# Performance work log

Measured on AMD Instinct MI355X. Metric: run time of the kernel, lower is better.

## Reference

```python
import jax, jax.numpy as jnp
import numpy as np

N, B, S, E, D, L, H, OUT = 16384, 32, 512, 262144, 256, 4, 4, 768
DH = D // H
ATOM_VOCABS = [119, 9, 12, 12, 10, 6, 9, 2, 2]
BOND_VOCABS = [22, 6, 2]
BN_EPS = 1e-5


def bn(x, g, b):
    # BatchNorm1d over nodes (training-mode statistics, deterministic)
    mu = x.mean(0)
    var = ((x - mu) ** 2).mean(0)
    return (x - mu) * jax.lax.rsqrt(var + BN_EPS) * g + b


def setup_inputs():
    key = jax.random.key(0)
    ks = iter(jax.random.split(key, 80))
    x = jnp.stack([jax.random.randint(next(ks), (N,), 0, v) for v in ATOM_VOCABS], 1)
    edge_attr = jnp.stack([jax.random.randint(next(ks), (E,), 0, v) for v in BOND_VOCABS], 1)
    epg = E // B  # edges per graph, edges stay within their graph
    gid = jnp.arange(E) // epg
    src = jax.random.randint(next(ks), (E,), 0, S) + gid * S
    dst = jax.random.randint(next(ks), (E,), 0, S) + gid * S
    edge_index = jnp.stack([src, dst], 0)
    batch_vec = jnp.arange(N) // S  # B equal-sized graphs, contiguous

    def rn(shape, std=0.02):
        return jax.random.normal(next(ks), shape, jnp.float32) * std

    inp = dict(x=x, edge_attr=edge_attr, edge_index=edge_index, batch_vec=batch_vec)
    inp['atom_tab'] = rn((len(ATOM_VOCABS), max(ATOM_VOCABS), D))
    inp['bond_tab'] = rn((len(BOND_VOCABS), max(BOND_VOCABS), D))
    inp['elin_w'] = rn((L, D, D)); inp['elin_b'] = jnp.zeros((L, D))
    inp['eps'] = jnp.zeros((L,))  # GINE train_eps init 0
    inp['gw1'] = rn((L, D, 2 * D)); inp['gb1'] = jnp.zeros((L, 2 * D))
    inp['gw2'] = rn((L, 2 * D, D)); inp['gb2'] = jnp.zeros((L, D))
    inp['aw_in'] = rn((L, D, 3 * D)); inp['ab_in'] = jnp.zeros((L, 3 * D))
    inp['aw_out'] = rn((L, D, D)); inp['ab_out'] = jnp.zeros((L, D))
    for n in ('n1', 'n2', 'n3'):
        inp[n + 'g'] = jnp.ones((L, D)); inp[n + 'b'] = jnp.zeros((L, D))
    inp['mw1'] = rn((L, D, 2 * D)); inp['mb1'] = jnp.zeros((L, 2 * D))
    inp['mw2'] = rn((L, 2 * D, D)); inp['mb2'] = jnp.zeros((L, D))
    inp['pw1'] = rn((D, D)); inp['pb1'] = jnp.zeros((D,))
    inp['pw2'] = rn((D, OUT)); inp['pb2'] = jnp.zeros((OUT,))
    return inp


def forward(x, edge_attr, edge_index, batch_vec, atom_tab, bond_tab, elin_w, elin_b, eps,
            gw1, gb1, gw2, gb2, aw_in, ab_in, aw_out, ab_out,
            n1g, n1b, n2g, n2b, n3g, n3b, mw1, mb1, mw2, mb2,
            pw1, pb1, pw2, pb2):
    # AtomEncoder / BondEncoder: sum of per-feature embeddings
    h = atom_tab[jnp.arange(atom_tab.shape[0])[None, :], x].sum(1)      # [N, D]
    e = bond_tab[jnp.arange(bond_tab.shape[0])[None, :], edge_attr].sum(1)  # [E, D]
    src, dst = edge_index[0], edge_index[1]
    scale = 1.0 / np.sqrt(DH)
    for l in range(L):
        # --- GINEConv local branch ---
        el = e @ elin_w[l] + elin_b[l]                       # edge lin
        msg = jax.nn.relu(h[src] + el)                       # [E, D]
        agg = jax.ops.segment_sum(msg, dst, num_segments=N)  # scatter-add
        hc = (1.0 + eps[l]) * h + agg
        hc = jax.nn.relu(hc @ gw1[l] + gb1[l]) @ gw2[l] + gb2[l]
        hc = bn(hc + h, n1g[l], n1b[l])
        # --- global multihead attention (dense per-graph batch, all slots valid) ---
        hd = h.reshape(B, S, D)
        qkv = hd @ aw_in[l] + ab_in[l]
        q, k, v = jnp.split(qkv, 3, axis=-1)
        q = q.reshape(B, S, H, DH).transpose(0, 2, 1, 3)
        k = k.reshape(B, S, H, DH).transpose(0, 2, 1, 3)
        v = v.reshape(B, S, H, DH).transpose(0, 2, 1, 3)
        attn = jax.nn.softmax(jnp.einsum('bhqd,bhkd->bhqk', q, k) * scale, axis=-1)
        ao = jnp.einsum('bhqk,bhkd->bhqd', attn, v).transpose(0, 2, 1, 3).reshape(N, D)
        ao = ao @ aw_out[l] + ab_out[l]
        ha = bn(ao + h, n2g[l], n2b[l])
        # --- combine + MLP ---
        out = hc + ha
        out = out + (jax.nn.relu(out @ mw1[l] + mb1[l]) @ mw2[l] + mb2[l])
        h = bn(out, n3g[l], n3b[l])
    # global mean pool
    counts = jax.ops.segment_sum(jnp.ones((N, 1), h.dtype), batch_vec, num_segments=B)
    g = jax.ops.segment_sum(h, batch_vec, num_segments=B) / counts
    z = jax.nn.relu(g @ pw1 + pb1) @ pw2 + pb2
    return z / jnp.linalg.norm(z, axis=-1, keepdims=True)


def reference(x, edge_attr, edge_index, batch_vec, atom_tab, bond_tab, elin_w, elin_b, eps,
              gw1, gb1, gw2, gb2, aw_in, ab_in, aw_out, ab_out,
              n1g, n1b, n2g, n2b, n3g, n3b, mw1, mb1, mw2, mb2,
              pw1, pb1, pw2, pb2):
    return forward(x, edge_attr, edge_index, batch_vec, atom_tab, bond_tab, elin_w, elin_b, eps,
                   gw1, gb1, gw2, gb2, aw_in, ab_in, aw_out, ab_out,
                   n1g, n1b, n2g, n2b, n3g, n3b, mw1, mb1, mw2, mb2,
                   pw1, pb1, pw2, pb2)
```

## Files before the change

kernel.cpp:

```cpp
#include <hip/hip_runtime.h>
#include <hip/hip_bf16.h>
#include <math.h>

#define N_NODES 16384
#define NB      32
#define S_PG    512
#define NE      262144
#define EPG     8192
#define D       256
#define D2      512
#define D3      768
#define NL      4
#define NH      4
#define DHD     64
#define OUTD    768
#define NCOMBO  264
#define WT_PER_LAYER 786432

typedef short s8v __attribute__((ext_vector_type(8)));
typedef float f4v __attribute__((ext_vector_type(4)));

__device__ __forceinline__ unsigned bfr(float f) {
    unsigned u = __float_as_uint(f);
    return (u + 0x7fffu + ((u >> 16) & 1u)) >> 16;
}
__device__ __forceinline__ float b2f(unsigned short u) {
    return __uint_as_float(((unsigned)u) << 16);
}

__global__ __launch_bounds__(256) void k_atom_enc(const int* __restrict__ x,
                                                  const float* __restrict__ tab,
                                                  float* __restrict__ h,
                                                  unsigned short* __restrict__ hb) {
    int node = blockIdx.x * 4 + (threadIdx.x >> 6);
    int lane = threadIdx.x & 63;
    int dd = lane << 2;
    float4 acc = {0.f, 0.f, 0.f, 0.f};
#pragma unroll
    for (int f = 0; f < 9; ++f) {
        int v = x[node * 9 + f];
        const float4 t = *(const float4*)&tab[((size_t)(f * 119 + v)) * D + dd];
        acc.x += t.x; acc.y += t.y; acc.z += t.z; acc.w += t.w;
    }
    *(float4*)&h[(size_t)node * D + dd] = acc;
    ushort4 o;
    o.x = (unsigned short)bfr(acc.x); o.y = (unsigned short)bfr(acc.y);
    o.z = (unsigned short)bfr(acc.z); o.w = (unsigned short)bfr(acc.w);
    *(ushort4*)&hb[(size_t)node * D + dd] = o;
}

__global__ __launch_bounds__(256) void k_bondw(const float* __restrict__ bond_tab,
                                               const float* __restrict__ elin_w,
                                               float* __restrict__ bw) {
    int blk = blockIdx.x;
    int l = blk / 66, fv = blk % 66;
    int dout = threadIdx.x;
    const float* tabrow = bond_tab + (size_t)fv * D;
    const float* w = elin_w + (size_t)l * D * D;
    float acc = 0.f;
    for (int d = 0; d < D; ++d) acc = fmaf(tabrow[d], w[d * D + dout], acc);
    bw[((size_t)l * 66 + fv) * D + dout] = acc;
}

__global__ __launch_bounds__(256) void k_combo(const float* __restrict__ bw,
                                               const float* __restrict__ elin_b,
                                               unsigned short* __restrict__ ctb) {
    int b = blockIdx.x;
    int l = b / NCOMBO, cid = b % NCOMBO;
    int a0 = cid / 12, a1 = (cid % 12) / 2, a2 = cid & 1;
    int d = threadIdx.x;
    const float* bwl = bw + (size_t)l * 66 * D;
    float v = bwl[(size_t)a0 * D + d] + bwl[(size_t)(22 + a1) * D + d] +
              bwl[(size_t)(44 + a2) * D + d] + elin_b[(size_t)l * D + d];
    ctb[((size_t)l * NCOMBO + cid) * D + d] = (unsigned short)bfr(v);
}

__global__ __launch_bounds__(256) void k_zero16k(int* __restrict__ p) {
    p[blockIdx.x * 256 + threadIdx.x] = 0;
}
__global__ __launch_bounds__(256) void k_zero_stats(float* __restrict__ p) {
    for (int i = 0; i < 6; ++i) p[i * 256 + threadIdx.x] = 0.f;
}
__global__ __launch_bounds__(256) void k_hist(const int* __restrict__ dst, int* __restrict__ deg) {
    int e = blockIdx.x * 256 + threadIdx.x;
    atomicAdd(&deg[dst[e]], 1);
}
__global__ __launch_bounds__(256) void k_scan(const int* __restrict__ deg,
                                              int* __restrict__ row_ptr,
                                              int* __restrict__ cursor) {
    __shared__ int partial[256];
    int t = threadIdx.x;
    int base = t * 64;
    int s = 0;
    for (int i = 0; i < 64; ++i) s += deg[base + i];
    partial[t] = s;
    __syncthreads();
    for (int dstp = 1; dstp < 256; dstp <<= 1) {
        int v = (t >= dstp) ? partial[t - dstp] : 0;
        __syncthreads();
        partial[t] += v;
        __syncthreads();
    }
    int run = partial[t] - s;
    for (int i = 0; i < 64; ++i) {
        int dcur = deg[base + i];
        row_ptr[base + i] = run;
        cursor[base + i] = run;
        run += dcur;
    }
    if (t == 255) row_ptr[N_NODES] = run;
}
__global__ __launch_bounds__(256) void k_scatter(const int* __restrict__ src,
                                                 const int* __restrict__ dst,
                                                 const int* __restrict__ ea,
                                                 int* __restrict__ cursor,
                                                 int2* __restrict__ sorted) {
    int e = blockIdx.x * 256 + threadIdx.x;
    int d = dst[e];
    int pos = atomicAdd(&cursor[d], 1);
    int cid = ea[e * 3] * 12 + ea[e * 3 + 1] * 2 + ea[e * 3 + 2];
    sorted[pos] = make_int2(src[e], cid);
}

__global__ __launch_bounds__(256) void k_gine_agg(const unsigned short* __restrict__ hb,
                                                  const float* __restrict__ h,
                                                  const unsigned short* __restrict__ ctb,
                                                  const float* __restrict__ eps, int l,
                                                  const int* __restrict__ row_ptr,
                                                  const int2* __restrict__ sorted,
                                                  unsigned short* __restrict__ aggb) {
    int w = threadIdx.x >> 6;
    int lane = threadIdx.x & 63;
    int n = blockIdx.x * 4 + w;
    int dd = lane << 2;
    int beg = row_ptr[n], end = row_ptr[n + 1];
    float4 acc = {0.f, 0.f, 0.f, 0.f};
    int i = beg;
    for (; i + 2 <= end; i += 2) {
        int2 e0 = sorted[i];
        int2 e1 = sorted[i + 1];
        ushort4 h0 = *(const ushort4*)&hb[(size_t)e0.x * D + dd];
        ushort4 c0 = *(const ushort4*)&ctb[(size_t)e0.y * D + dd];
        ushort4 h1 = *(const ushort4*)&hb[(size_t)e1.x * D + dd];
        ushort4 c1 = *(const ushort4*)&ctb[(size_t)e1.y * D + dd];
        acc.x += fmaxf(b2f(h0.x) + b2f(c0.x), 0.f) + fmaxf(b2f(h1.x) + b2f(c1.x), 0.f);
        acc.y += fmaxf(b2f(h0.y) + b2f(c0.y), 0.f) + fmaxf(b2f(h1.y) + b2f(c1.y), 0.f);
        acc.z += fmaxf(b2f(h0.z) + b2f(c0.z), 0.f) + fmaxf(b2f(h1.z) + b2f(c1.z), 0.f);
        acc.w += fmaxf(b2f(h0.w) + b2f(c0.w), 0.f) + fmaxf(b2f(h1.w) + b2f(c1.w), 0.f);
    }
    if (i < end) {
        int2 e0 = sorted[i];
        ushort4 h0 = *(const ushort4*)&hb[(size_t)e0.x * D + dd];
        ushort4 c0 = *(const ushort4*)&ctb[(size_t)e0.y * D + dd];
        acc.x += fmaxf(b2f(h0.x) + b2f(c0.x), 0.f);
        acc.y += fmaxf(b2f(h0.y) + b2f(c0.y), 0.f);
        acc.z += fmaxf(b2f(h0.z) + b2f(c0.z), 0.f);
        acc.w += fmaxf(b2f(h0.w) + b2f(c0.w), 0.f);
    }
    float s1p = 1.f + eps[l];
    float4 hn = *(const float4*)&h[(size_t)n * D + dd];
    ushort4 o;
    o.x = (unsigned short)bfr(s1p * hn.x + acc.x);
    o.y = (unsigned short)bfr(s1p * hn.y + acc.y);
    o.z = (unsigned short)bfr(s1p * hn.z + acc.z);
    o.w = (unsigned short)bfr(s1p * hn.w + acc.w);
    *(ushort4*)&aggb[(size_t)n * D + dd] = o;
}

__global__ __launch_bounds__(256) void k_wcvt(const float* __restrict__ gw1, const float* __restrict__ gw2,
                                              const float* __restrict__ aw_in, const float* __restrict__ aw_out,
                                              const float* __restrict__ mw1, const float* __restrict__ mw2,
                                              unsigned short* __restrict__ WT) {
    const int KS[6]   = {256, 512, 256, 256, 256, 512};
    const int NS[6]   = {512, 256, 768, 256, 512, 256};
    const int TOFF[7] = {0, 128, 256, 448, 512, 640, 768};
    const int DOFF[6] = {0, 131072, 262144, 458752, 524288, 655360};
    int b = blockIdx.x;
    int l = b / 768, wb = b % 768;
    int widx = 0;
    while (wb >= TOFF[widx + 1]) ++widx;
    int t = wb - TOFF[widx];
    int K = KS[widx], N = NS[widx];
    int nn = N / 32;
    int kt = t / nn, nt = t % nn;
    const float* srcs[6] = {gw1, gw2, aw_in, aw_out, mw1, mw2};
    const float* W = srcs[widx] + (size_t)l * K * N;
    unsigned short* WTp = WT + (size_t)l * WT_PER_LAYER + DOFF[widx];
    __shared__ float tile[32][33];
    int tid = threadIdx.x;
    int r = tid >> 3, c4 = (tid & 7) << 2;
    float4 v = *(const float4*)&W[(size_t)(kt * 32 + r) * N + nt * 32 + c4];
    tile[r][c4] = v.x; tile[r][c4 + 1] = v.y; tile[r][c4 + 2] = v.z; tile[r][c4 + 3] = v.w;
    __syncthreads();
    int nr = tid >> 3, kc = (tid & 7) << 2;
    ushort4 o;
    o.x = (unsigned short)bfr(tile[kc + 0][nr]);
    o.y = (unsigned short)bfr(tile[kc + 1][nr]);
    o.z = (unsigned short)bfr(tile[kc + 2][nr]);
    o.w = (unsigned short)bfr(tile[kc + 3][nr]);
    *(ushort4*)&WTp[(size_t)(nt * 32 + nr) * K + kt * 32 + kc] = o;
}

template<int RELU, int RES, int OBF, int STAT>
__global__ __launch_bounds__(256) void k_mm2(const unsigned short* __restrict__ A,
                                             const unsigned short* __restrict__ BT,
                                             const float* __restrict__ bias,
                                             const float* __restrict__ res,
                                             void* __restrict__ Cp,
                                             float* __restrict__ stat,
                                             int M, int N, int K) {
    __shared__ unsigned short As[128 * 64];
    __shared__ unsigned short Bs[128 * 64];
    const int tid = threadIdx.x;
    const int row0 = blockIdx.y * 128, col0 = blockIdx.x * 128;
    const int w = tid >> 6, l = tid & 63;
    const int wm = w >> 1, wn = w & 1;
    const int lr = l & 15, lq = l >> 4;
    const int srow = l >> 3;
    const int scol = (l & 7) * 8;
    f4v acc[4][4] = {};

    const unsigned short* Ag = A + (size_t)(row0 + w * 32 + srow) * K + scol;
    const unsigned short* Bg = BT + (size_t)(col0 + w * 32 + srow) * K + scol;
    unsigned short* Al = &As[(w * 32) * 64];
    unsigned short* Bl = &Bs[(w * 32) * 64];

    for (int k0 = 0; k0 < K; k0 += 64) {
#pragma unroll
        for (int it = 0; it < 4; ++it) {
            __builtin_amdgcn_global_load_lds(
                (const __attribute__((address_space(1))) unsigned*)(Ag + (size_t)(it * 8) * K + k0),
                (__attribute__((address_space(3))) unsigned*)(Al + it * 8 * 64), 16, 0, 0);
            __builtin_amdgcn_global_load_lds(
                (const __attribute__((address_space(1))) unsigned*)(Bg + (size_t)(it * 8) * K + k0),
                (__attribute__((address_space(3))) unsigned*)(Bl + it * 8 * 64), 16, 0, 0);
        }
        asm volatile("s_waitcnt vmcnt(0)" ::: "memory");
        __syncthreads();
#pragma unroll
        for (int kk = 0; kk < 2; ++kk) {
            s8v af[4], bf[4];
#pragma unroll
            for (int m = 0; m < 4; ++m)
                af[m] = *(const s8v*)&As[(wm * 64 + m * 16 + lr) * 64 + kk * 32 + lq * 8];
#pragma unroll
            for (int n = 0; n < 4; ++n)
                bf[n] = *(const s8v*)&Bs[(wn * 64 + n * 16 + lr) * 64 + kk * 32 + lq * 8];
#pragma unroll
            for (int m = 0; m < 4; ++m)
#pragma unroll
                for (int n = 0; n < 4; ++n)
                    acc[m][n] = __builtin_amdgcn_mfma_f32_16x16x32_bf16(af[m], bf[n], acc[m][n], 0, 0, 0);
        }
        __syncthreads();
    }
    float cs[4], cs2[4];
#pragma unroll
    for (int n = 0; n < 4; ++n) { cs[n] = 0.f; cs2[n] = 0.f; }
#pragma unroll
    for (int n = 0; n < 4; ++n) {
        int c = col0 + wn * 64 + n * 16 + lr;
        float bv = bias[c];
#pragma unroll
        for (int m = 0; m < 4; ++m) {
#pragma unroll
            for (int j = 0; j < 4; ++j) {
                int r = row0 + wm * 64 + m * 16 + lq * 4 + j;
                float v = acc[m][n][j] + bv;
                if (RES) v += res[(size_t)r * N + c];
                if (STAT) { cs[n] += v; cs2[n] += v * v; }
                if (RELU) v = fmaxf(v, 0.f);
                if (OBF) ((unsigned short*)Cp)[(size_t)r * N + c] = (unsigned short)bfr(v);
                else ((float*)Cp)[(size_t)r * N + c] = v;
            }
        }
    }
    if (STAT) {
#pragma unroll
        for (int n = 0; n < 4; ++n) {
            float s = cs[n], s2 = cs2[n];
            s += __shfl_xor(s, 16);  s2 += __shfl_xor(s2, 16);
            s += __shfl_xor(s, 32);  s2 += __shfl_xor(s2, 32);
            if (lq == 0) {
                int c = col0 + wn * 64 + n * 16 + lr;
                atomicAdd(&stat[c], s);
                atomicAdd(&stat[256 + c], s2);
            }
        }
    }
}

__global__ __launch_bounds__(256) void k_mm2_dual(const unsigned short* __restrict__ A1,
                                                  const unsigned short* __restrict__ B1,
                                                  const float* __restrict__ bias1,
                                                  unsigned short* __restrict__ C1, int N1, int nb1,
                                                  const unsigned short* __restrict__ A2,
                                                  const unsigned short* __restrict__ B2,
                                                  const float* __restrict__ bias2,
                                                  unsigned short* __restrict__ C2, int N2,
                                                  int K) {
    __shared__ unsigned short As[128 * 64];
    __shared__ unsigned short Bs[128 * 64];
    const unsigned short* A; const unsigned short* BT; const float* bias;
    unsigned short* C; int N, cb, relu;
    if ((int)blockIdx.x < nb1) { A = A1; BT = B1; bias = bias1; C = C1; N = N1; cb = blockIdx.x; relu = 1; }
    else { A = A2; BT = B2; bias = bias2; C = C2; N = N2; cb = blockIdx.x - nb1; relu = 0; }
    const int tid = threadIdx.x;
    const int row0 = blockIdx.y * 128, col0 = cb * 128;
    const int w = tid >> 6, l = tid & 63;
    const int wm = w >> 1, wn = w & 1;
    const int lr = l & 15, lq = l >> 4;
    const int srow = l >> 3;
    const int scol = (l & 7) * 8;
    f4v acc[4][4] = {};

    const unsigned short* Ag = A + (size_t)(row0 + w * 32 + srow) * K + scol;
    const unsigned short* Bg = BT + (size_t)(col0 + w * 32 + srow) * K + scol;
    unsigned short* Al = &As[(w * 32) * 64];
    unsigned short* Bl = &Bs[(w * 32) * 64];

    for (int k0 = 0; k0 < K; k0 += 64) {
#pragma unroll
        for (int it = 0; it < 4; ++it) {
            __builtin_amdgcn_global_load_lds(
                (const __attribute__((address_space(1))) unsigned*)(Ag + (size_t)(it * 8) * K + k0),
                (__attribute__((address_space(3))) unsigned*)(Al + it * 8 * 64), 16, 0, 0);
            __builtin_amdgcn_global_load_lds(
                (const __attribute__((address_space(1))) unsigned*)(Bg + (size_t)(it * 8) * K + k0),
                (__attribute__((address_space(3))) unsigned*)(Bl + it * 8 * 64), 16, 0, 0);
        }
        asm volatile("s_waitcnt vmcnt(0)" ::: "memory");
        __syncthreads();
#pragma unroll
        for (int kk = 0; kk < 2; ++kk) {
            s8v af[4], bf[4];
#pragma unroll
            for (int m = 0; m < 4; ++m)
                af[m] = *(const s8v*)&As[(wm * 64 + m * 16 + lr) * 64 + kk * 32 + lq * 8];
#pragma unroll
            for (int n = 0; n < 4; ++n)
                bf[n] = *(const s8v*)&Bs[(wn * 64 + n * 16 + lr) * 64 + kk * 32 + lq * 8];
#pragma unroll
            for (int m = 0; m < 4; ++m)
#pragma unroll
                for (int n = 0; n < 4; ++n)
                    acc[m][n] = __builtin_amdgcn_mfma_f32_16x16x32_bf16(af[m], bf[n], acc[m][n], 0, 0, 0);
        }
        __syncthreads();
    }
#pragma unroll
    for (int n = 0; n < 4; ++n) {
        int c = col0 + wn * 64 + n * 16 + lr;
        float bv = bias[c];
#pragma unroll
        for (int m = 0; m < 4; ++m) {
#pragma unroll
            for (int j = 0; j < 4; ++j) {
                int r = row0 + wm * 64 + m * 16 + lq * 4 + j;
                float v = acc[m][n][j] + bv;
                if (relu) v = fmaxf(v, 0.f);
                C[(size_t)r * N + c] = (unsigned short)bfr(v);
            }
        }
    }
}

template<int RELU, int RES, int OBF, int STAT>
__global__ __launch_bounds__(256) void k_mm64(const unsigned short* __restrict__ A,
                                              const unsigned short* __restrict__ BT,
                                              const float* __restrict__ bias,
                                              const float* __restrict__ res,
                                              void* __restrict__ Cp,
                                              float* __restrict__ stat,
                                              int M, int N, int K) {
    __shared__ unsigned short As[64 * 64];
    __shared__ unsigned short Bs[128 * 64];
    const int tid = threadIdx.x;
    const int row0 = blockIdx.y * 64, col0 = blockIdx.x * 128;
    const int w = tid >> 6, l = tid & 63;
    const int wn = w;
    const int lr = l & 15, lq = l >> 4;
    const int srow = l >> 3;
    const int scol = (l & 7) * 8;
    f4v acc[4][2] = {};

    const unsigned short* Ag = A + (size_t)(row0 + w * 16 + srow) * K + scol;
    const unsigned short* Bg = BT + (size_t)(col0 + w * 32 + srow) * K + scol;
    unsigned short* Al = &As[(w * 16) * 64];
    unsigned short* Bl = &Bs[(w * 32) * 64];

    for (int k0 = 0; k0 < K; k0 += 64) {
#pragma unroll
        for (int it = 0; it < 2; ++it)
            __builtin_amdgcn_global_load_lds(
                (const __attribute__((address_space(1))) unsigned*)(Ag + (size_t)(it * 8) * K + k0),
                (__attribute__((address_space(3))) unsigned*)(Al + it * 8 * 64), 16, 0, 0);
#pragma unroll
        for (int it = 0; it < 4; ++it)
            __builtin_amdgcn_global_load_lds(
                (const __attribute__((address_space(1))) unsigned*)(Bg + (size_t)(it * 8) * K + k0),
                (__attribute__((address_space(3))) unsigned*)(Bl + it * 8 * 64), 16, 0, 0);
        asm volatile("s_waitcnt vmcnt(0)" ::: "memory");
        __syncthreads();
#pragma unroll
        for (int kk = 0; kk < 2; ++kk) {
            s8v af[4], bf[2];
#pragma unroll
            for (int m = 0; m < 4; ++m)
                af[m] = *(const s8v*)&As[(m * 16 + lr) * 64 + kk * 32 + lq * 8];
#pragma unroll
            for (int n = 0; n < 2; ++n)
                bf[n] = *(const s8v*)&Bs[(wn * 32 + n * 16 + lr) * 64 + kk * 32 + lq * 8];
#pragma unroll
            for (int m = 0; m < 4; ++m)
#pragma unroll
                for (int n = 0; n < 2; ++n)
                    acc[m][n] = __builtin_amdgcn_mfma_f32_16x16x32_bf16(af[m], bf[n], acc[m][n], 0, 0, 0);
        }
        __syncthreads();
    }
    float cs[2], cs2[2];
#pragma unroll
    for (int n = 0; n < 2; ++n) { cs[n] = 0.f; cs2[n] = 0.f; }
#pragma unroll
    for (int n = 0; n < 2; ++n) {
        int c = col0 + wn * 32 + n * 16 + lr;
        float bv = bias[c];
#pragma unroll
        for (int m = 0; m < 4; ++m) {
#pragma unroll
            for (int j = 0; j < 4; ++j) {
                int r = row0 + m * 16 + lq * 4 + j;
                float v = acc[m][n][j] + bv;
                if (RES) v += res[(size_t)r * N + c];
                if (STAT) { cs[n] += v; cs2[n] += v * v; }
                if (RELU) v = fmaxf(v, 0.f);
                if (OBF) ((unsigned short*)Cp)[(size_t)r * N + c] = (unsigned short)bfr(v);
                else ((float*)Cp)[(size_t)r * N + c] = v;
            }
        }
    }
    if (STAT) {
#pragma unroll
        for (int n = 0; n < 2; ++n) {
            float s = cs[n], s2 = cs2[n];
            s += __shfl_xor(s, 16);  s2 += __shfl_xor(s2, 16);
            s += __shfl_xor(s, 32);  s2 += __shfl_xor(s2, 32);
            if (lq == 0) {
                int c = col0 + wn * 32 + n * 16 + lr;
                atomicAdd(&stat[c], s);
                atomicAdd(&stat[256 + c], s2);
            }
        }
    }
}

__global__ __launch_bounds__(256) void k_bn_finish(float* __restrict__ acc,
                                                   float* __restrict__ ms) {
    int c = threadIdx.x;
    float s = acc[c], s2 = acc[256 + c];
    float mean = s / (float)N_NODES;
    float var = s2 / (float)N_NODES - mean * mean;
    ms[c] = mean;
    ms[D + c] = rsqrtf(var + 1e-5f);
    acc[c] = 0.f;
    acc[256 + c] = 0.f;
}
__global__ __launch_bounds__(256) void k_bn_finish2(float* __restrict__ acc,
                                                    float* __restrict__ ms) {
    int s0 = blockIdx.x;
    float* a = acc + (size_t)s0 * 512;
    float* m = ms + (size_t)s0 * 2 * D;
    int c = threadIdx.x;
    float s = a[c], s2 = a[256 + c];
    float mean = s / (float)N_NODES;
    float var = s2 / (float)N_NODES - mean * mean;
    m[c] = mean;
    m[D + c] = rsqrtf(var + 1e-5f);
    a[c] = 0.f;
    a[256 + c] = 0.f;
}

__global__ __launch_bounds__(256) void k_bn12(const float* __restrict__ t1,
                                              const float* __restrict__ ms1,
                                              const float* __restrict__ g1,
                                              const float* __restrict__ b1,
                                              const float* __restrict__ t2,
                                              const float* __restrict__ ms2,
                                              const float* __restrict__ g2,
                                              const float* __restrict__ b2,
                                              float* __restrict__ y,
                                              unsigned short* __restrict__ yb) {
    size_t i4 = (size_t)blockIdx.x * blockDim.x + threadIdx.x;
    int c = (int)((i4 & 63) << 2);
    float4 v1 = ((const float4*)t1)[i4];
    float4 v2 = ((const float4*)t2)[i4];
    float4 v;
    v.x = (v1.x - ms1[c + 0]) * ms1[D + c + 0] * g1[c + 0] + b1[c + 0]
        + (v2.x - ms2[c + 0]) * ms2[D + c + 0] * g2[c + 0] + b2[c + 0];
    v.y = (v1.y - ms1[c + 1]) * ms1[D + c + 1] * g1[c + 1] + b1[c + 1]
        + (v2.y - ms2[c + 1]) * ms2[D + c + 1] * g2[c + 1] + b2[c + 1];
    v.z = (v1.z - ms1[c + 2]) * ms1[D + c + 2] * g1[c + 2] + b1[c + 2]
        + (v2.z - ms2[c + 2]) * ms2[D + c + 2] * g2[c + 2] + b2[c + 2];
    v.w = (v1.w - ms1[c + 3]) * ms1[D + c + 3] * g1[c + 3] + b1[c + 3]
        + (v2.w - ms2[c + 3]) * ms2[D + c + 3] * g2[c + 3] + b2[c + 3];
    ((float4*)y)[i4] = v;
    ushort4 o;
    o.x = (unsigned short)bfr(v.x); o.y = (unsigned short)bfr(v.y);
    o.z = (unsigned short)bfr(v.z); o.w = (unsigned short)bfr(v.w);
    ((ushort4*)yb)[i4] = o;
}

__global__ __launch_bounds__(256) void k_bn_apply(const float* __restrict__ x,
                                                  const float* __restrict__ ms,
                                                  const float* __restrict__ g,
                                                  const float* __restrict__ b,
                                                  float* __restrict__ y,
                                                  unsigned short* __restrict__ yb) {
    size_t i4 = (size_t)blockIdx.x * blockDim.x + threadIdx.x;
    int c = (int)((i4 & 63) << 2);
    float4 v = ((const float4*)x)[i4];
    v.x = (v.x - ms[c + 0]) * ms[D + c + 0] * g[c + 0] + b[c + 0];
    v.y = (v.y - ms[c + 1]) * ms[D + c + 1] * g[c + 1] + b[c + 1];
    v.z = (v.z - ms[c + 2]) * ms[D + c + 2] * g[c + 2] + b[c + 2];
    v.w = (v.w - ms[c + 3]) * ms[D + c + 3] * g[c + 3] + b[c + 3];
    ((float4*)y)[i4] = v;
    ushort4 o;
    o.x = (unsigned short)bfr(v.x); o.y = (unsigned short)bfr(v.y);
    o.z = (unsigned short)bfr(v.z); o.w = (unsigned short)bfr(v.w);
    ((ushort4*)yb)[i4] = o;
}

__global__ __launch_bounds__(256) void k_flash_mfma(const unsigned short* __restrict__ qkv,
                                                    unsigned short* __restrict__ ao) {
    __shared__ unsigned short Ks[64][72];
    __shared__ unsigned short VT[64][72];
    __shared__ unsigned short Ps[4][16][72];
    const int bh = blockIdx.x;
    const int b = bh >> 2, hh = bh & 3;
    const int i0 = blockIdx.y << 6;
    const int tid = threadIdx.x;
    const int w = tid >> 6, l = tid & 63;
    const int lr = l & 15, lq = l >> 4;
    const int hd = hh * DHD;
    const size_t rowbase = (size_t)(b * S_PG) * D3;

    s8v aq[2];
    {
        const unsigned short* qrow = &qkv[rowbase + (size_t)(i0 + w * 16 + lr) * D3 + hd + lq * 8];
        aq[0] = *(const s8v*)&qrow[0];
        aq[1] = *(const s8v*)&qrow[32];
    }

    float mrow[4] = {-INFINITY, -INFINITY, -INFINITY, -INFINITY};
    float lrow[4] = {0.f, 0.f, 0.f, 0.f};
    f4v oacc[4] = {};

    const int skv = tid >> 2;
    const int sd0 = (tid & 3) << 4;
    const int d0v = (tid >> 4) << 2;
    const int kv0 = (tid & 15) << 2;

    for (int j0 = 0; j0 < S_PG; j0 += 64) {
        __syncthreads();
        {
            const unsigned short* kr = &qkv[rowbase + (size_t)(j0 + skv) * D3 + D + hd + sd0];
            *(uint4*)&Ks[skv][sd0]     = *(const uint4*)&kr[0];
            *(uint4*)&Ks[skv][sd0 + 8] = *(const uint4*)&kr[8];
            unsigned short vv[4][4];
#pragma unroll
            for (int i = 0; i < 4; ++i) {
                uint2 lv = *(const uint2*)&qkv[rowbase + (size_t)(j0 + kv0 + i) * D3 + D2 + hd + d0v];
                vv[i][0] = (unsigned short)(lv.x & 0xffffu);
                vv[i][1] = (unsigned short)(lv.x >> 16);
                vv[i][2] = (unsigned short)(lv.y & 0xffffu);
                vv[i][3] = (unsigned short)(lv.y >> 16);
            }
#pragma unroll
            for (int i2 = 0; i2 < 4; ++i2) {
                ushort4 o4;
                o4.x = vv[0][i2]; o4.y = vv[1][i2]; o4.z = vv[2][i2]; o4.w = vv[3][i2];
                *(ushort4*)&VT[d0v + i2][kv0] = o4;
            }
        }
        __syncthreads();
        f4v sc[4] = {};
#pragma unroll
        for (int nt = 0; nt < 4; ++nt) {
            s8v bk0 = *(const s8v*)&Ks[nt * 16 + lr][lq * 8];
            s8v bk1 = *(const s8v*)&Ks[nt * 16 + lr][32 + lq * 8];
            sc[nt] = __builtin_amdgcn_mfma_f32_16x16x32_bf16(aq[0], bk0, sc[nt], 0, 0, 0);
            sc[nt] = __builtin_amdgcn_mfma_f32_16x16x32_bf16(aq[1], bk1, sc[nt], 0, 0, 0);
        }
        float ps[4][4], alpha[4];
#pragma unroll
        for (int j = 0; j < 4; ++j) {
#pragma unroll
            for (int nt = 0; nt < 4; ++nt) ps[nt][j] = sc[nt][j] * 0.125f;
            float pm = fmaxf(fmaxf(ps[0][j], ps[1][j]), fmaxf(ps[2][j], ps[3][j]));
#pragma unroll
            for (int off = 1; off < 16; off <<= 1) pm = fmaxf(pm, __shfl_xor(pm, off));
            float mn = fmaxf(mrow[j], pm);
            alpha[j] = __expf(mrow[j] - mn);
            float rs = 0.f;
#pragma unroll
            for (int nt = 0; nt < 4; ++nt) { ps[nt][j] = __expf(ps[nt][j] - mn); rs += ps[nt][j]; }
#pragma unroll
            for (int off = 1; off < 16; off <<= 1) rs += __shfl_xor(rs, off);
            lrow[j] = lrow[j] * alpha[j] + rs;
            mrow[j] = mn;
        }
#pragma unroll
        for (int nt = 0; nt < 4; ++nt)
#pragma unroll
            for (int j = 0; j < 4; ++j)
                Ps[w][lq * 4 + j][nt * 16 + lr] = (unsigned short)bfr(ps[nt][j]);
#pragma unroll
        for (int ntd = 0; ntd < 4; ++ntd)
#pragma unroll
            for (int j = 0; j < 4; ++j) oacc[ntd][j] *= alpha[j];
        s8v pa0 = *(const s8v*)&Ps[w][lr][lq * 8];
        s8v pa1 = *(const s8v*)&Ps[w][lr][32 + lq * 8];
#pragma unroll
        for (int ntd = 0; ntd < 4; ++ntd) {
            s8v bv0 = *(const s8v*)&VT[ntd * 16 + lr][lq * 8];
            s8v bv1 = *(const s8v*)&VT[ntd * 16 + lr][32 + lq * 8];
            oacc[ntd] = __builtin_amdgcn_mfma_f32_16x16x32_bf16(pa0, bv0, oacc[ntd], 0, 0, 0);
            oacc[ntd] = __builtin_amdgcn_mfma_f32_16x16x32_bf16(pa1, bv1, oacc[ntd], 0, 0, 0);
        }
    }
#pragma unroll
    for (int j = 0; j < 4; ++j) {
        float inv = 1.f / lrow[j];
        int node = b * S_PG + i0 + w * 16 + lq * 4 + j;
#pragma unroll
        for (int ntd = 0; ntd < 4; ++ntd)
            ao[(size_t)node * D + hd + ntd * 16 + lr] = (unsigned short)bfr(oacc[ntd][j] * inv);
    }
}

__global__ __launch_bounds__(256) void k_pool(const float* __restrict__ h, float* __restrict__ g) {
    int b = blockIdx.x, c = threadIdx.x;
    const float* p = h + (size_t)b * S_PG * D + c;
    float s = 0.f;
    for (int r = 0; r < S_PG; ++r) s += p[(size_t)r * D];
    g[b * D + c] = s * (1.f / (float)S_PG);
}

__global__ __launch_bounds__(256) void k_final(const float* __restrict__ g,
                                               const float* __restrict__ pw1,
                                               const float* __restrict__ pb1,
                                               const float* __restrict__ pw2,
                                               const float* __restrict__ pb2,
                                               float* __restrict__ out) {
    __shared__ float gs[D];
    __shared__ float ts[D];
    __shared__ float red[4];
    int b = blockIdx.x, tid = threadIdx.x;
    gs[tid] = g[b * D + tid];
    __syncthreads();
    float acc = pb1[tid];
    for (int d = 0; d < D; ++d) acc = fmaf(gs[d], pw1[d * D + tid], acc);
    ts[tid] = fmaxf(acc, 0.f);
    __syncthreads();
    float z[3];
#pragma unroll
    for (int rep = 0; rep < 3; ++rep) {
        int j = tid + rep * 256;
        float a = pb2[j];
        for (int d = 0; d < D; ++d) a = fmaf(ts[d], pw2[(size_t)d * OUTD + j], a);
        z[rep] = a;
    }
    float ss = z[0] * z[0] + z[1] * z[1] + z[2] * z[2];
#pragma unroll
    for (int o = 32; o >= 1; o >>= 1) ss += __shfl_xor(ss, o);
    if ((tid & 63) == 0) red[tid >> 6] = ss;
    __syncthreads();
    float rn = rsqrtf(red[0] + red[1] + red[2] + red[3]);
#pragma unroll
    for (int rep = 0; rep < 3; ++rep) out[b * OUTD + tid + rep * 256] = z[rep] * rn;
}

extern "C" void kernel_launch(void* const* d_in, const int* in_sizes, int n_in,
                              void* d_out, int out_size, void* d_ws, size_t ws_size,
                              hipStream_t stream) {
    const int* x        = (const int*)d_in[0];
    const int* ea       = (const int*)d_in[1];
    const int* eidx     = (const int*)d_in[2];
    const float* atom_tab = (const float*)d_in[4];
    const float* bond_tab = (const float*)d_in[5];
    const float* elin_w = (const float*)d_in[6];
    const float* elin_b = (const float*)d_in[7];
    const float* eps    = (const float*)d_in[8];
    const float* gw1    = (const float*)d_in[9];
    const float* gb1    = (const float*)d_in[10];
    const float* gw2    = (const float*)d_in[11];
    const float* gb2    = (const float*)d_in[12];
    const float* aw_in  = (const float*)d_in[13];
    const float* ab_in  = (const float*)d_in[14];
    const float* aw_out = (const float*)d_in[15];
    const float* ab_out = (const float*)d_in[16];
    const float* n1g    = (const float*)d_in[17];
    const float* n1b    = (const float*)d_in[18];
    const float* n2g    = (const float*)d_in[19];
    const float* n2b    = (const float*)d_in[20];
    const float* n3g    = (const float*)d_in[21];
    const float* n3b    = (const float*)d_in[22];
    const float* mw1    = (const float*)d_in[23];
    const float* mb1    = (const float*)d_in[24];
    const float* mw2    = (const float*)d_in[25];
    const float* mb2    = (const float*)d_in[26];
    const float* pw1    = (const float*)d_in[27];
    const float* pb1    = (const float*)d_in[28];
    const float* pw2    = (const float*)d_in[29];
    const float* pb2    = (const float*)d_in[30];

    char* ws = (char*)d_ws;
    size_t off = 0;
    auto alloc = [&](size_t bytes) {
        void* p = ws + off;
        off += (bytes + 255) & ~(size_t)255;
        return p;
    };
    float*  h    = (float*)alloc((size_t)N_NODES * D * 4);
    float*  bufB = (float*)alloc((size_t)N_NODES * D * 4);
    float*  tmp1 = (float*)alloc((size_t)N_NODES * D * 4);
    unsigned short* hb = (unsigned short*)alloc((size_t)N_NODES * D * 2);
    char*   U    = (char*)alloc((size_t)N_NODES * D3 * 2);
    unsigned short* bfA = (unsigned short*)alloc((size_t)N_NODES * D3 * 2);
    unsigned short* WT  = (unsigned short*)alloc((size_t)NL * WT_PER_LAYER * 2);
    float*  bw   = (float*)alloc((size_t)NL * 66 * D * 4);
    unsigned short* ctb = (unsigned short*)alloc((size_t)NL * NCOMBO * D * 2);
    int*    deg  = (int*)alloc((size_t)N_NODES * 4);
    int*    row_ptr = (int*)alloc((size_t)(N_NODES + 1) * 4);
    int*    cursor  = (int*)alloc((size_t)N_NODES * 4);
    int2*   sorted  = (int2*)alloc((size_t)NE * 8);
    float*  statacc = (float*)alloc((size_t)3 * 512 * 4);
    float*  msbuf   = (float*)alloc((size_t)3 * 2 * D * 4);
    float*  g    = (float*)alloc((size_t)NB * D * 4);
    (void)ws_size; (void)in_sizes; (void)n_in; (void)out_size;

    float* tmp23 = (float*)U;
    unsigned short* qkv = (unsigned short*)U;
    unsigned short* aggb  = bfA;
    unsigned short* ao    = bfA;
    unsigned short* bufBb = bfA;
    unsigned short* hid   = bfA + (size_t)N_NODES * D;
    float* ms1 = msbuf, *ms3 = msbuf + 4 * D;

    const int* srcp = eidx;
    const int* dstp = eidx + NE;
    const int EW = N_NODES * D / 1024;

    k_zero16k<<<N_NODES / 256, 256, 0, stream>>>(deg);
    k_zero_stats<<<1, 256, 0, stream>>>(statacc);
    k_hist<<<NE / 256, 256, 0, stream>>>(dstp, deg);
    k_scan<<<1, 256, 0, stream>>>(deg, row_ptr, cursor);
    k_scatter<<<NE / 256, 256, 0, stream>>>(srcp, dstp, ea, cursor, sorted);
    k_atom_enc<<<N_NODES / 4, 256, 0, stream>>>(x, atom_tab, h, hb);
    k_bondw<<<NL * 66, 256, 0, stream>>>(bond_tab, elin_w, bw);
    k_combo<<<NL * NCOMBO, 256, 0, stream>>>(bw, elin_b, ctb);
    k_wcvt<<<NL * 768, 256, 0, stream>>>(gw1, gw2, aw_in, aw_out, mw1, mw2, WT);

    for (int l = 0; l < NL; ++l) {
        const unsigned short* WTl = WT + (size_t)l * WT_PER_LAYER;
        k_gine_agg<<<N_NODES / 4, 256, 0, stream>>>(hb, h, ctb + (size_t)l * NCOMBO * D, eps, l,
                                                    row_ptr, sorted, aggb);
        k_mm2_dual<<<dim3(10, N_NODES / 128), 256, 0, stream>>>(
            aggb, WTl + 0, gb1 + (size_t)l * D2, hid, D2, 4,
            hb, WTl + 262144, ab_in + (size_t)l * D3, qkv, D3, D);
        k_mm64<0, 1, 0, 1><<<dim3(D / 128, N_NODES / 64), 256, 0, stream>>>(
            hid, WTl + 131072, gb2 + (size_t)l * D, h, tmp1, statacc, N_NODES, D, D2);
        k_flash_mfma<<<dim3(NB * NH, S_PG / 64), 256, 0, stream>>>(qkv, ao);
        k_mm64<0, 1, 0, 1><<<dim3(D / 128, N_NODES / 64), 256, 0, stream>>>(
            ao, WTl + 458752, ab_out + (size_t)l * D, h, tmp23, statacc + 512, N_NODES, D, D);
        k_bn_finish2<<<2, 256, 0, stream>>>(statacc, msbuf);
        k_bn12<<<EW, 256, 0, stream>>>(tmp1, ms1, n1g + l * D, n1b + l * D,
                                       tmp23, msbuf + 2 * D, n2g + l * D, n2b + l * D, bufB, bufBb);
        k_mm2<1, 0, 1, 0><<<dim3(D2 / 128, N_NODES / 128), 256, 0, stream>>>(
            bufBb, WTl + 524288, mb1 + (size_t)l * D2, nullptr, hid, nullptr, N_NODES, D2, D);
        k_mm64<0, 1, 0, 1><<<dim3(D / 128, N_NODES / 64), 256, 0, stream>>>(
            hid, WTl + 655360, mb2 + (size_t)l * D, bufB, tmp23, statacc + 1024, N_NODES, D, D2);
        k_bn_finish<<<1, 256, 0, stream>>>(statacc + 1024, ms3);
        k_bn_apply<<<EW, 256, 0, stream>>>(tmp23, ms3, n3g + l * D, n3b + l * D, h, hb);
    }
    k_pool<<<NB, 256, 0, stream>>>(h, g);
    k_final<<<NB, 256, 0, stream>>>(g, pw1, pb1, pw2, pb2, (float*)d_out);
}
```

Measured before the change: 942.9 us.

## Fuse dual residual GEMMs, inline BN finalize, and widen flash-attention query tiles

Merges the two 256-wide residual GEMMs (GINE second layer and attention output projection) into one dual launch so their tiles run concurrently. The separate BN-finish kernels are removed: each layer gets its own zeroed stat slot, and the apply kernels compute mean and rsqrt inline from the accumulated sums. Flash attention now processes 128 queries per block (two 64-row groups per wave), so each loaded K/V tile is reused twice. This cuts launches and K/V reloads, at the cost of recomputing rsqrt per element and more registers in the attention kernel.

```diff
diff --git a/kernel.cpp b/kernel.cpp
--- a/kernel.cpp
+++ b/kernel.cpp
@@ -16,6 +16,7 @@
 #define OUTD    768
 #define NCOMBO  264
 #define WT_PER_LAYER 786432
+#define INV_N   (1.0f / (float)N_NODES)
 
 typedef short s8v __attribute__((ext_vector_type(8)));
 typedef float f4v __attribute__((ext_vector_type(4)));
@@ -78,8 +79,8 @@
 __global__ __launch_bounds__(256) void k_zero16k(int* __restrict__ p) {
     p[blockIdx.x * 256 + threadIdx.x] = 0;
 }
-__global__ __launch_bounds__(256) void k_zero_stats(float* __restrict__ p) {
-    for (int i = 0; i < 6; ++i) p[i * 256 + threadIdx.x] = 0.f;
+__global__ __launch_bounds__(256) void k_zero_stats12(float* __restrict__ p) {
+    for (int i = 0; i < 24; ++i) p[i * 256 + threadIdx.x] = 0.f;
 }
 __global__ __launch_bounds__(256) void k_hist(const int* __restrict__ dst, int* __restrict__ deg) {
     int e = blockIdx.x * 256 + threadIdx.x;
@@ -455,106 +456,183 @@
     }
 }
 
-__global__ __launch_bounds__(256) void k_bn_finish(float* __restrict__ acc,
-                                                   float* __restrict__ ms) {
-    int c = threadIdx.x;
-    float s = acc[c], s2 = acc[256 + c];
-    float mean = s / (float)N_NODES;
-    float var = s2 / (float)N_NODES - mean * mean;
-    ms[c] = mean;
-    ms[D + c] = rsqrtf(var + 1e-5f);
-    acc[c] = 0.f;
-    acc[256 + c] = 0.f;
-}
-__global__ __launch_bounds__(256) void k_bn_finish2(float* __restrict__ acc,
-                                                    float* __restrict__ ms) {
-    int s0 = blockIdx.x;
-    float* a = acc + (size_t)s0 * 512;
-    float* m = ms + (size_t)s0 * 2 * D;
-    int c = threadIdx.x;
-    float s = a[c], s2 = a[256 + c];
-    float mean = s / (float)N_NODES;
-    float var = s2 / (float)N_NODES - mean * mean;
-    m[c] = mean;
-    m[D + c] = rsqrtf(var + 1e-5f);
-    a[c] = 0.f;
-    a[256 + c] = 0.f;
-}
-
-__global__ __launch_bounds__(256) void k_bn12(const float* __restrict__ t1,
-                                              const float* __restrict__ ms1,
-                                              const float* __restrict__ g1,
-                                              const float* __restrict__ b1,
-                                              const float* __restrict__ t2,
-                                              const float* __restrict__ ms2,
-                                              const float* __restrict__ g2,
-                                              const float* __restrict__ b2,
-                                              float* __restrict__ y,
-                                              unsigned short* __restrict__ yb) {
+__global__ __launch_bounds__(256) void k_mm64_dual(const unsigned short* __restrict__ A1,
+                                                   const unsigned short* __restrict__ B1,
+                                                   const float* __restrict__ bias1,
+                                                   const float* __restrict__ res1,
+                                                   float* __restrict__ C1,
+                                                   float* __restrict__ stat1, int K1, int nb1,
+                                                   const unsigned short* __restrict__ A2,
+                                                   const unsigned short* __restrict__ B2,
+                                                   const float* __restrict__ bias2,
+                                                   const float* __restrict__ res2,
+                                                   float* __restrict__ C2,
+                                                   float* __restrict__ stat2, int K2) {
+    __shared__ unsigned short As[64 * 64];
+    __shared__ unsigned short Bs[128 * 64];
+    const unsigned short *A, *BT; const float *bias, *res; float *C, *stat;
+    int K, cb;
+    if ((int)blockIdx.x < nb1) { A = A1; BT = B1; bias = bias1; res = res1; C = C1; stat = stat1; K = K1; cb = blockIdx.x; }
+    else { A = A2; BT = B2; bias = bias2; res = res2; C = C2; stat = stat2; K = K2; cb = blockIdx.x - nb1; }
+    const int N = 256;
+    const int tid = threadIdx.x;
+    const int row0 = blockIdx.y * 64, col0 = cb * 128;
+    const int w = tid >> 6, l = tid & 63;
+    const int wn = w;
+    const int lr = l & 15, lq = l >> 4;
+    const int srow = l >> 3;
+    const int scol = (l & 7) * 8;
+    f4v acc[4][2] = {};
+
+    const unsigned short* Ag = A + (size_t)(row0 + w * 16 + srow) * K + scol;
+    const unsigned short* Bg = BT + (size_t)(col0 + w * 32 + srow) * K + scol;
+    unsigned short* Al = &As[(w * 16) * 64];
+    unsigned short* Bl = &Bs[(w * 32) * 64];
+
+    for (int k0 = 0; k0 < K; k0 += 64) {
+#pragma unroll
+        for (int it = 0; it < 2; ++it)
+            __builtin_amdgcn_global_load_lds(
+                (const __attribute__((address_space(1))) unsigned*)(Ag + (size_t)(it * 8) * K + k0),
+                (__attribute__((address_space(3))) unsigned*)(Al + it * 8 * 64), 16, 0, 0);
+#pragma unroll
+        for (int it = 0; it < 4; ++it)
+            __builtin_amdgcn_global_load_lds(
+                (const __attribute__((address_space(1))) unsigned*)(Bg + (size_t)(it * 8) * K + k0),
+                (__attribute__((address_space(3))) unsigned*)(Bl + it * 8 * 64), 16, 0, 0);
+        asm volatile("s_waitcnt vmcnt(0)" ::: "memory");
+        __syncthreads();
+#pragma unroll
+        for (int kk = 0; kk < 2; ++kk) {
+            s8v af[4], bf[2];
+#pragma unroll
+            for (int m = 0; m < 4; ++m)
+                af[m] = *(const s8v*)&As[(m * 16 + lr) * 64 + kk * 32 + lq * 8];
+#pragma unroll
+            for (int n = 0; n < 2; ++n)
+                bf[n] = *(const s8v*)&Bs[(wn * 32 + n * 16 + lr) * 64 + kk * 32 + lq * 8];
+#pragma unroll
+            for (int m = 0; m < 4; ++m)
+#pragma unroll
+                for (int n = 0; n < 2; ++n)
+                    acc[m][n] = __builtin_amdgcn_mfma_f32_16x16x32_bf16(af[m], bf[n], acc[m][n], 0, 0, 0);
+        }
+        __syncthreads();
+    }
+    float cs[2], cs2[2];
+#pragma unroll
+    for (int n = 0; n < 2; ++n) { cs[n] = 0.f; cs2[n] = 0.f; }
+#pragma unroll
+    for (int n = 0; n < 2; ++n) {
+        int c = col0 + wn * 32 + n * 16 + lr;
+        float bv = bias[c];
+#pragma unroll
+        for (int m = 0; m < 4; ++m) {
+#pragma unroll
+            for (int j = 0; j < 4; ++j) {
+                int r = row0 + m * 16 + lq * 4 + j;
+                float v = acc[m][n][j] + bv + res[(size_t)r * N + c];
+                cs[n] += v; cs2[n] += v * v;
+                C[(size_t)r * N + c] = v;
+            }
+        }
+    }
+#pragma unroll
+    for (int n = 0; n < 2; ++n) {
+        float s = cs[n], s2 = cs2[n];
+        s += __shfl_xor(s, 16);  s2 += __shfl_xor(s2, 16);
+        s += __shfl_xor(s, 32);  s2 += __shfl_xor(s2, 32);
+        if (lq == 0) {
+            int c = col0 + wn * 32 + n * 16 + lr;
+            atomicAdd(&stat[c], s);
+            atomicAdd(&stat[256 + c], s2);
+        }
+    }
+}
+
+__global__ __launch_bounds__(256) void k_bn12i(const float* __restrict__ t1,
+                                               const float* __restrict__ sa1,
+                                               const float* __restrict__ g1,
+                                               const float* __restrict__ b1,
+                                               const float* __restrict__ t2,
+                                               const float* __restrict__ sa2,
+                                               const float* __restrict__ g2,
+                                               const float* __restrict__ b2,
+                                               float* __restrict__ y,
+                                               unsigned short* __restrict__ yb) {
     size_t i4 = (size_t)blockIdx.x * blockDim.x + threadIdx.x;
     int c = (int)((i4 & 63) << 2);
-    float4 v1 = ((const float4*)t1)[i4];
-    float4 v2 = ((const float4*)t2)[i4];
-    float4 v;
-    v.x = (v1.x - ms1[c + 0]) * ms1[D + c + 0] * g1[c + 0] + b1[c + 0]
-        + (v2.x - ms2[c + 0]) * ms2[D + c + 0] * g2[c + 0] + b2[c + 0];
-    v.y = (v1.y - ms1[c + 1]) * ms1[D + c + 1] * g1[c + 1] + b1[c + 1]
-        + (v2.y - ms2[c + 1]) * ms2[D + c + 1] * g2[c + 1] + b2[c + 1];
-    v.z = (v1.z - ms1[c + 2]) * ms1[D + c + 2] * g1[c + 2] + b1[c + 2]
-        + (v2.z - ms2[c + 2]) * ms2[D + c + 2] * g2[c + 2] + b2[c + 2];
-    v.w = (v1.w - ms1[c + 3]) * ms1[D + c + 3] * g1[c + 3] + b1[c + 3]
-        + (v2.w - ms2[c + 3]) * ms2[D + c + 3] * g2[c + 3] + b2[c + 3];
-    ((float4*)y)[i4] = v;
-    ushort4 o;
-    o.x = (unsigned short)bfr(v.x); o.y = (unsigned short)bfr(v.y);
-    o.z = (unsigned short)bfr(v.z); o.w = (unsigned short)bfr(v.w);
-    ((ushort4*)yb)[i4] = o;
-}
-
-__global__ __launch_bounds__(256) void k_bn_apply(const float* __restrict__ x,
-                                                  const float* __restrict__ ms,
-                                                  const float* __restrict__ g,
-                                                  const float* __restrict__ b,
-                                                  float* __restrict__ y,
-                                                  unsigned short* __restrict__ yb) {
+    float a1[4], a2[4], o[4];
+    *(float4*)a1 = ((const float4*)t1)[i4];
+    *(float4*)a2 = ((const float4*)t2)[i4];
+#pragma unroll
+    for (int q = 0; q < 4; ++q) {
+        int cc = c + q;
+        float m1 = sa1[cc] * INV_N;
+        float r1 = rsqrtf(sa1[256 + cc] * INV_N - m1 * m1 + 1e-5f);
+        float m2 = sa2[cc] * INV_N;
+        float r2 = rsqrtf(sa2[256 + cc] * INV_N - m2 * m2 + 1e-5f);
+        o[q] = (a1[q] - m1) * r1 * g1[cc] + b1[cc] + (a2[q] - m2) * r2 * g2[cc] + b2[cc];
+    }
+    ((float4*)y)[i4] = *(float4*)o;
+    ushort4 ob;
+    ob.x = (unsigned short)bfr(o[0]); ob.y = (unsigned short)bfr(o[1]);
+    ob.z = (unsigned short)bfr(o[2]); ob.w = (unsigned short)bfr(o[3]);
+    ((ushort4*)yb)[i4] = ob;
+}
+
+__global__ __launch_bounds__(256) void k_bn_apply_i(const float* __restrict__ x,
+                                                    const float* __restrict__ sa,
+                                                    const float* __restrict__ g,
+                                                    const float* __restrict__ b,
+                                                    float* __restrict__ y,
+                                                    unsigned short* __restrict__ yb) {
     size_t i4 = (size_t)blockIdx.x * blockDim.x + threadIdx.x;
     int c = (int)((i4 & 63) << 2);
-    float4 v = ((const float4*)x)[i4];
-    v.x = (v.x - ms[c + 0]) * ms[D + c + 0] * g[c + 0] + b[c + 0];
-    v.y = (v.y - ms[c + 1]) * ms[D + c + 1] * g[c + 1] + b[c + 1];
-    v.z = (v.z - ms[c + 2]) * ms[D + c + 2] * g[c + 2] + b[c + 2];
-    v.w = (v.w - ms[c + 3]) * ms[D + c + 3] * g[c + 3] + b[c + 3];
-    ((float4*)y)[i4] = v;
-    ushort4 o;
-    o.x = (unsigned short)bfr(v.x); o.y = (unsigned short)bfr(v.y);
-    o.z = (unsigned short)bfr(v.z); o.w = (unsigned short)bfr(v.w);
-    ((ushort4*)yb)[i4] = o;
+    float a[4], o[4];
+    *(float4*)a = ((const float4*)x)[i4];
+#pragma unroll
+    for (int q = 0; q < 4; ++q) {
+        int cc = c + q;
+        float m = sa[cc] * INV_N;
+        float r = rsqrtf(sa[256 + cc] * INV_N - m * m + 1e-5f);
+        o[q] = (a[q] - m) * r * g[cc] + b[cc];
+    }
+    ((float4*)y)[i4] = *(float4*)o;
+    ushort4 ob;
+    ob.x = (unsigned short)bfr(o[0]); ob.y = (unsigned short)bfr(o[1]);
+    ob.z = (unsigned short)bfr(o[2]); ob.w = (unsigned short)bfr(o[3]);
+    ((ushort4*)yb)[i4] = ob;
 }
 
 __global__ __launch_bounds__(256) void k_flash_mfma(const unsigned short* __restrict__ qkv,
                                                     unsigned short* __restrict__ ao) {
     __shared__ unsigned short Ks[64][72];
     __shared__ unsigned short VT[64][72];
-    __shared__ unsigned short Ps[4][16][72];
+    __shared__ unsigned short Ps[4][2][16][72];
     const int bh = blockIdx.x;
     const int b = bh >> 2, hh = bh & 3;
-    const int i0 = blockIdx.y << 6;
+    const int i0 = blockIdx.y << 7;
     const int tid = threadIdx.x;
     const int w = tid >> 6, l = tid & 63;
     const int lr = l & 15, lq = l >> 4;
     const int hd = hh * DHD;
     const size_t rowbase = (size_t)(b * S_PG) * D3;
 
-    s8v aq[2];
-    {
-        const unsigned short* qrow = &qkv[rowbase + (size_t)(i0 + w * 16 + lr) * D3 + hd + lq * 8];
-        aq[0] = *(const s8v*)&qrow[0];
-        aq[1] = *(const s8v*)&qrow[32];
-    }
-
-    float mrow[4] = {-INFINITY, -INFINITY, -INFINITY, -INFINITY};
-    float lrow[4] = {0.f, 0.f, 0.f, 0.f};
-    f4v oacc[4] = {};
+    s8v aq[2][2];
+#pragma unroll
+    for (int g = 0; g < 2; ++g) {
+        const unsigned short* qrow = &qkv[rowbase + (size_t)(i0 + g * 64 + w * 16 + lr) * D3 + hd + lq * 8];
+        aq[g][0] = *(const s8v*)&qrow[0];
+        aq[g][1] = *(const s8v*)&qrow[32];
+    }
+
+    float mrow[2][4], lrow[2][4];
+    f4v oacc[2][4] = {};
+#pragma unroll
+    for (int g = 0; g < 2; ++g)
+#pragma unroll
+        for (int j = 0; j < 4; ++j) { mrow[g][j] = -INFINITY; lrow[g][j] = 0.f; }
 
     const int skv = tid >> 2;
     const int sd0 = (tid & 3) << 4;
@@ -584,59 +662,64 @@
             }
         }
         __syncthreads();
-        f4v sc[4] = {};
-#pragma unroll
-        for (int nt = 0; nt < 4; ++nt) {
-            s8v bk0 = *(const s8v*)&Ks[nt * 16 + lr][lq * 8];
-            s8v bk1 = *(const s8v*)&Ks[nt * 16 + lr][32 + lq * 8];
-            sc[nt] = __builtin_amdgcn_mfma_f32_16x16x32_bf16(aq[0], bk0, sc[nt], 0, 0, 0);
-            sc[nt] = __builtin_amdgcn_mfma_f32_16x16x32_bf16(aq[1], bk1, sc[nt], 0, 0, 0);
-        }
-        float ps[4][4], alpha[4];
+#pragma unroll
+        for (int g = 0; g < 2; ++g) {
+            f4v sc[4] = {};
+#pragma unroll
+            for (int nt = 0; nt < 4; ++nt) {
+                s8v bk0 = *(const s8v*)&Ks[nt * 16 + lr][lq * 8];
+                s8v bk1 = *(const s8v*)&Ks[nt * 16 + lr][32 + lq * 8];
+                sc[nt] = __builtin_amdgcn_mfma_f32_16x16x32_bf16(aq[g][0], bk0, sc[nt], 0, 0, 0);
+                sc[nt] = __builtin_amdgcn_mfma_f32_16x16x32_bf16(aq[g][1], bk1, sc[nt], 0, 0, 0);
+            }
+            float ps[4][4], alpha[4];
+#pragma unroll
+            for (int j = 0; j < 4; ++j) {
+#pragma unroll
+                for (int nt = 0; nt < 4; ++nt) ps[nt][j] = sc[nt][j] * 0.125f;
+                float pm = fmaxf(fmaxf(ps[0][j], ps[1][j]), fmaxf(ps[2][j], ps[3][j]));
+#pragma unroll
+                for (int off = 1; off < 16; off <<= 1) pm = fmaxf(pm, __shfl_xor(pm, off));
+                float mn = fmaxf(mrow[g][j], pm);
+                alpha[j] = __expf(mrow[g][j] - mn);
+                float rs = 0.f;
+#pragma unroll
+                for (int nt = 0; nt < 4; ++nt) { ps[nt][j] = __expf(ps[nt][j] - mn); rs += ps[nt][j]; }
+#pragma unroll
+                for (int off = 1; off < 16; off <<= 1) rs += __shfl_xor(rs, off);
+                lrow[g][j] = lrow[g][j] * alpha[j] + rs;
+                mrow[g][j] = mn;
+            }
+#pragma unroll
+            for (int nt = 0; nt < 4; ++nt)
+#pragma unroll
+                for (int j = 0; j < 4; ++j)
+                    Ps[w][g][lq * 4 + j][nt * 16 + lr] = (unsigned short)bfr(ps[nt][j]);
+#pragma unroll
+            for (int ntd = 0; ntd < 4; ++ntd)
+#pragma unroll
+                for (int j = 0; j < 4; ++j) oacc[g][ntd][j] *= alpha[j];
+            s8v pa0 = *(const s8v*)&Ps[w][g][lr][lq * 8];
+            s8v pa1 = *(const s8v*)&Ps[w][g][lr][32 + lq * 8];
+#pragma unroll
+            for (int ntd = 0; ntd < 4; ++ntd) {
+                s8v bv0 = *(const s8v*)&VT[ntd * 16 + lr][lq * 8];
+                s8v bv1 = *(const s8v*)&VT[ntd * 16 + lr][32 + lq * 8];
+                oacc[g][ntd] = __builtin_amdgcn_mfma_f32_16x16x32_bf16(pa0, bv0, oacc[g][ntd], 0, 0, 0);
+                oacc[g][ntd] = __builtin_amdgcn_mfma_f32_16x16x32_bf16(pa1, bv1, oacc[g][ntd], 0, 0, 0);
+            }
+        }
+    }
+#pragma unroll
+    for (int g = 0; g < 2; ++g)
 #pragma unroll
         for (int j = 0; j < 4; ++j) {
-#pragma unroll
-            for (int nt = 0; nt < 4; ++nt) ps[nt][j] = sc[nt][j] * 0.125f;
-            float pm = fmaxf(fmaxf(ps[0][j], ps[1][j]), fmaxf(ps[2][j], ps[3][j]));
-#pragma unroll
-            for (int off = 1; off < 16; off <<= 1) pm = fmaxf(pm, __shfl_xor(pm, off));
-            float mn = fmaxf(mrow[j], pm);
-            alpha[j] = __expf(mrow[j] - mn);
-            float rs = 0.f;
-#pragma unroll
-            for (int nt = 0; nt < 4; ++nt) { ps[nt][j] = __expf(ps[nt][j] - mn); rs += ps[nt][j]; }
-#pragma unroll
-            for (int off = 1; off < 16; off <<= 1) rs += __shfl_xor(rs, off);
-            lrow[j] = lrow[j] * alpha[j] + rs;
-            mrow[j] = mn;
-        }
-#pragma unroll
-        for (int nt = 0; nt < 4; ++nt)
-#pragma unroll
-            for (int j = 0; j < 4; ++j)
-                Ps[w][lq * 4 + j][nt * 16 + lr] = (unsigned short)bfr(ps[nt][j]);
-#pragma unroll
-        for (int ntd = 0; ntd < 4; ++ntd)
-#pragma unroll
-            for (int j = 0; j < 4; ++j) oacc[ntd][j] *= alpha[j];
-        s8v pa0 = *(const s8v*)&Ps[w][lr][lq * 8];
-        s8v pa1 = *(const s8v*)&Ps[w][lr][32 + lq * 8];
-#pragma unroll
-        for (int ntd = 0; ntd < 4; ++ntd) {
-            s8v bv0 = *(const s8v*)&VT[ntd * 16 + lr][lq * 8];
-            s8v bv1 = *(const s8v*)&VT[ntd * 16 + lr][32 + lq * 8];
-            oacc[ntd] = __builtin_amdgcn_mfma_f32_16x16x32_bf16(pa0, bv0, oacc[ntd], 0, 0, 0);
-            oacc[ntd] = __builtin_amdgcn_mfma_f32_16x16x32_bf16(pa1, bv1, oacc[ntd], 0, 0, 0);
-        }
-    }
-#pragma unroll
-    for (int j = 0; j < 4; ++j) {
-        float inv = 1.f / lrow[j];
-        int node = b * S_PG + i0 + w * 16 + lq * 4 + j;
-#pragma unroll
-        for (int ntd = 0; ntd < 4; ++ntd)
-            ao[(size_t)node * D + hd + ntd * 16 + lr] = (unsigned short)bfr(oacc[ntd][j] * inv);
-    }
+            float inv = 1.f / lrow[g][j];
+            int node = b * S_PG + i0 + g * 64 + w * 16 + lq * 4 + j;
+#pragma unroll
+            for (int ntd = 0; ntd < 4; ++ntd)
+                ao[(size_t)node * D + hd + ntd * 16 + lr] = (unsigned short)bfr(oacc[g][ntd][j] * inv);
+        }
 }
 
 __global__ __launch_bounds__(256) void k_pool(const float* __restrict__ h, float* __restrict__ g) {
@@ -735,8 +818,7 @@
     int*    row_ptr = (int*)alloc((size_t)(N_NODES + 1) * 4);
     int*    cursor  = (int*)alloc((size_t)N_NODES * 4);
     int2*   sorted  = (int2*)alloc((size_t)NE * 8);
-    float*  statacc = (float*)alloc((size_t)3 * 512 * 4);
-    float*  msbuf   = (float*)alloc((size_t)3 * 2 * D * 4);
+    float*  statacc = (float*)alloc((size_t)12 * 512 * 4);
     float*  g    = (float*)alloc((size_t)NB * D * 4);
     (void)ws_size; (void)in_sizes; (void)n_in; (void)out_size;
 
@@ -746,14 +828,13 @@
     unsigned short* ao    = bfA;
     unsigned short* bufBb = bfA;
     unsigned short* hid   = bfA + (size_t)N_NODES * D;
-    float* ms1 = msbuf, *ms3 = msbuf + 4 * D;
 
     const int* srcp = eidx;
     const int* dstp = eidx + NE;
     const int EW = N_NODES * D / 1024;
 
     k_zero16k<<<N_NODES / 256, 256, 0, stream>>>(deg);
-    k_zero_stats<<<1, 256, 0, stream>>>(statacc);
+    k_zero_stats12<<<1, 256, 0, stream>>>(statacc);
     k_hist<<<NE / 256, 256, 0, stream>>>(dstp, deg);
     k_scan<<<1, 256, 0, stream>>>(deg, row_ptr, cursor);
     k_scatter<<<NE / 256, 256, 0, stream>>>(srcp, dstp, ea, cursor, sorted);
@@ -764,25 +845,25 @@
 
     for (int l = 0; l < NL; ++l) {
         const unsigned short* WTl = WT + (size_t)l * WT_PER_LAYER;
+        float* sl0 = statacc + (size_t)(l * 3 + 0) * 512;
+        float* sl1 = statacc + (size_t)(l * 3 + 1) * 512;
+        float* sl2 = statacc + (size_t)(l * 3 + 2) * 512;
         k_gine_agg<<<N_NODES / 4, 256, 0, stream>>>(hb, h, ctb + (size_t)l * NCOMBO * D, eps, l,
                                                     row_ptr, sorted, aggb);
         k_mm2_dual<<<dim3(10, N_NODES / 128), 256, 0, stream>>>(
             aggb, WTl + 0, gb1 + (size_t)l * D2, hid, D2, 4,
             hb, WTl + 262144, ab_in + (size_t)l * D3, qkv, D3, D);
-        k_mm64<0, 1, 0, 1><<<dim3(D / 128, N_NODES / 64), 256, 0, stream>>>(
-            hid, WTl + 131072, gb2 + (size_t)l * D, h, tmp1, statacc, N_NODES, D, D2);
-        k_flash_mfma<<<dim3(NB * NH, S_PG / 64), 256, 0, stream>>>(qkv, ao);
-        k_mm64<0, 1, 0, 1><<<dim3(D / 128, N_NODES / 64), 256, 0, stream>>>(
-            ao, WTl + 458752, ab_out + (size_t)l * D, h, tmp23, statacc + 512, N_NODES, D, D);
-        k_bn_finish2<<<2, 256, 0, stream>>>(statacc, msbuf);
-        k_bn12<<<EW, 256, 0, stream>>>(tmp1, ms1, n1g + l * D, n1b + l * D,
-                                       tmp23, msbuf + 2 * D, n2g + l * D, n2b + l * D, bufB, bufBb);
+        k_flash_mfma<<<dim3(NB * NH, S_PG / 128), 256, 0, stream>>>(qkv, ao);
+        k_mm64_dual<<<dim3(4, N_NODES / 64), 256, 0, stream>>>(
+            hid, WTl + 131072, gb2 + (size_t)l * D, h, tmp1, sl0, D2, 2,
+            ao, WTl + 458752, ab_out + (size_t)l * D, h, tmp23, sl1, D);
+        k_bn12i<<<EW, 256, 0, stream>>>(tmp1, sl0, n1g + l * D, n1b + l * D,
+                                        tmp23, sl1, n2g + l * D, n2b + l * D, bufB, bufBb);
         k_mm2<1, 0, 1, 0><<<dim3(D2 / 128, N_NODES / 128), 256, 0, stream>>>(
             bufBb, WTl + 524288, mb1 + (size_t)l * D2, nullptr, hid, nullptr, N_NODES, D2, D);
         k_mm64<0, 1, 0, 1><<<dim3(D / 128, N_NODES / 64), 256, 0, stream>>>(
-            hid, WTl + 655360, mb2 + (size_t)l * D, bufB, tmp23, statacc + 1024, N_NODES, D, D2);
-        k_bn_finish<<<1, 256, 0, stream>>>(statacc + 1024, ms3);
-        k_bn_apply<<<EW, 256, 0, stream>>>(tmp23, ms3, n3g + l * D, n3b + l * D, h, hb);
+            hid, WTl + 655360, mb2 + (size_t)l * D, bufB, tmp23, sl2, N_NODES, D, D2);
+        k_bn_apply_i<<<EW, 256, 0, stream>>>(tmp23, sl2, n3g + l * D, n3b + l * D, h, hb);
     }
     k_pool<<<NB, 256, 0, stream>>>(h, g);
     k_final<<<NB, 256, 0, stream>>>(g, pw1, pb1, pw2, pb2, (float*)d_out);
```

After: 909.2 us. 1.04x faster.
